# Optimization experiments

Measured on AMD Instinct MI355X. Metric: run time of the kernel, lower is better.

Reference implementation:

```python
import jax, jax.numpy as jnp
import numpy as np

BINS = 10

def setup_inputs() -> dict:
    key = jax.random.key(0)
    k1, k2, k3 = jax.random.split(key, 3)
    B, C, H, W = 16, 80, 128, 128
    # predictions strictly inside (0,1) so log(pre) / log(1-pre) are finite
    pre = jax.random.uniform(k1, (B, C, H, W), dtype=jnp.float32) * 0.998 + 1e-3
    u = jax.random.uniform(k2, (B, C, H, W), dtype=jnp.float32)
    gt = jnp.where(u > 0.99, jnp.float32(1.0), u * 0.5).astype(jnp.float32)
    # accumulated per-bin sample counts (GHM running stats); strictly positive
    acc_sum = jax.random.uniform(k3, (BINS,), dtype=jnp.float32) * 1e5 + 1e3
    return {"pre": pre, "gt": gt, "acc_sum": acc_sum}

def reference(pre, gt, acc_sum):
    bins = acc_sum.shape[0]
    tot = pre.size  # B*C*H*W, python int
    # gradient magnitude, detached (torch: .detach())
    g = jax.lax.stop_gradient(jnp.abs(pre - gt))
    # edges[i] = i/bins with edges[-1] += 1e-6, so bin(g) = min(floor(g*bins), bins-1)
    bin_idx = jnp.clip(jnp.floor(g * bins).astype(jnp.int32), 0, bins - 1)
    counts = jnp.zeros((bins,), jnp.float32).at[bin_idx].add(1.0)  # histogram
    nonempty = counts > 0
    n = jnp.sum(nonempty.astype(jnp.float32))  # number of non-empty bins
    w_per_bin = jnp.where(nonempty, tot / acc_sum, jnp.float32(0.0))
    weights = w_per_bin[bin_idx]                       # scatter-style weight assignment
    weights = jnp.where(n > 0, weights / n, weights)
    pos_mask = (gt == 1.0).astype(pre.dtype)
    neg_mask = 1.0 - pos_mask
    loss = (jnp.log(pre) * pos_mask + jnp.log1p(-pre) * neg_mask) * weights
    return jnp.sum(loss) / tot
```

## Files before the change

kernel.cpp:

```cpp
#include <hip/hip_runtime.h>

#define BINS 10
#define NTHR 256
#define MAXBLK 2048
#define UNROLL 5


__device__ __forceinline__ void ghm_elem(float pe, float te,
                                         const float* __restrict__ wtab,
                                         float& acc, unsigned int& mask) {
    float g = fabsf(pe - te);
    int bin = (int)(g * 10.0f);
    bin = bin > (BINS - 1) ? (BINS - 1) : bin;
    mask |= (1u << bin);
    float arg = (te == 1.0f) ? pe : (1.0f - pe);
    acc = fmaf(__log2f(arg), wtab[bin], acc);
}

__global__ __launch_bounds__(NTHR) void ghm_partial_kernel(
    const float* __restrict__ pre,
    const float* __restrict__ gt,
    const float* __restrict__ acc_sum,
    float* __restrict__ blk_sum,
    unsigned int* __restrict__ blk_mask,
    int n4,
    int tot)
{
    __shared__ float wtab[BINS];
    if (threadIdx.x < BINS)
        wtab[threadIdx.x] = 0.69314718055994531f / acc_sum[threadIdx.x];
    __syncthreads();

    float acc0 = 0.0f, acc1 = 0.0f;
    unsigned int mask = 0u;

    const float4* __restrict__ p4 = reinterpret_cast<const float4*>(pre);
    const float4* __restrict__ g4 = reinterpret_cast<const float4*>(gt);

    const int stride = gridDim.x * blockDim.x;
    int i = blockIdx.x * blockDim.x + threadIdx.x;

    for (; i + (UNROLL - 1) * stride < n4; i += UNROLL * stride) {
        float4 P[UNROLL], T[UNROLL];
#pragma unroll
        for (int u = 0; u < UNROLL; ++u) {
            P[u] = p4[i + u * stride];
            T[u] = g4[i + u * stride];
        }
#pragma unroll
        for (int u = 0; u < UNROLL; ++u) {
            ghm_elem(P[u].x, T[u].x, wtab, acc0, mask);
            ghm_elem(P[u].y, T[u].y, wtab, acc1, mask);
            ghm_elem(P[u].z, T[u].z, wtab, acc0, mask);
            ghm_elem(P[u].w, T[u].w, wtab, acc1, mask);
        }
    }
    for (; i < n4; i += stride) {
        float4 p = p4[i];
        float4 t = g4[i];
        ghm_elem(p.x, t.x, wtab, acc0, mask);
        ghm_elem(p.y, t.y, wtab, acc1, mask);
        ghm_elem(p.z, t.z, wtab, acc0, mask);
        ghm_elem(p.w, t.w, wtab, acc1, mask);
    }
    const int rs = n4 * 4;
    const int rem = tot - rs;
    if (blockIdx.x == 0 && (int)threadIdx.x < rem) {
        ghm_elem(pre[rs + threadIdx.x], gt[rs + threadIdx.x], wtab, acc0, mask);
    }

    float acc = acc0 + acc1;

#pragma unroll
    for (int off = 32; off >= 1; off >>= 1) {
        acc  += __shfl_down(acc, off, 64);
        mask |= (unsigned int)__shfl_down((int)mask, off, 64);
    }

    __shared__ float ls[4];
    __shared__ unsigned int lm[4];
    const int lane = threadIdx.x & 63;
    const int wave = threadIdx.x >> 6;
    if (lane == 0) { ls[wave] = acc; lm[wave] = mask; }
    __syncthreads();
    if (threadIdx.x == 0) {
        blk_sum[blockIdx.x]  = ls[0] + ls[1] + ls[2] + ls[3];
        blk_mask[blockIdx.x] = lm[0] | lm[1] | lm[2] | lm[3];
    }
}

__global__ __launch_bounds__(NTHR) void ghm_finalize_kernel(
    const float* __restrict__ blk_sum,
    const unsigned int* __restrict__ blk_mask,
    float* __restrict__ out,
    int nblk)
{
    float acc = 0.0f;
    unsigned int mask = 0u;
    for (int i = threadIdx.x; i < nblk; i += NTHR) {
        acc  += blk_sum[i];
        mask |= blk_mask[i];
    }
#pragma unroll
    for (int off = 32; off >= 1; off >>= 1) {
        acc  += __shfl_down(acc, off, 64);
        mask |= (unsigned int)__shfl_down((int)mask, off, 64);
    }
    __shared__ float ls[4];
    __shared__ unsigned int lm[4];
    const int lane = threadIdx.x & 63;
    const int wave = threadIdx.x >> 6;
    if (lane == 0) { ls[wave] = acc; lm[wave] = mask; }
    __syncthreads();
    if (threadIdx.x == 0) {
        float total = ls[0] + ls[1] + ls[2] + ls[3];
        unsigned int m = lm[0] | lm[1] | lm[2] | lm[3];
        int n = __popc(m & ((1u << BINS) - 1u));
        out[0] = (n > 0) ? (total / (float)n) : total;
    }
}

extern "C" void kernel_launch(void* const* d_in, const int* in_sizes, int n_in,
                              void* d_out, int out_size, void* d_ws, size_t ws_size,
                              hipStream_t stream) {
    const float* pre     = (const float*)d_in[0];
    const float* gt      = (const float*)d_in[1];
    const float* acc_sum = (const float*)d_in[2];
    float* out = (float*)d_out;

    const int tot = in_sizes[0];
    const int n4  = tot / 4;

    int blocks = (n4 + NTHR - 1) / NTHR;
    if (blocks > MAXBLK) blocks = MAXBLK;
    if (blocks < 1) blocks = 1;

    float* blk_sum = (float*)d_ws;
    unsigned int* blk_mask = (unsigned int*)((char*)d_ws + MAXBLK * sizeof(float));

    ghm_partial_kernel<<<blocks, NTHR, 0, stream>>>(
        pre, gt, acc_sum, blk_sum, blk_mask, n4, tot);
    ghm_finalize_kernel<<<1, NTHR, 0, stream>>>(
        blk_sum, blk_mask, out, blocks);
}
```

Baseline: 188.7 us.

## Use contiguous per-block chunks with nontemporal vector loads, drop manual unroll

Replaces the grid-stride loop, which was unrolled five ways, with contiguous per-block chunks walked by a simple strided loop. Loads go through nontemporal builtins on ext_vector float4 types, hinting that the streamed data need not stay in cache. This aims to improve DRAM locality and cut cache pollution. The cost is less memory-level parallelism per thread, since the explicit five-way unroll that kept ten loads in flight is gone.

```diff
diff --git a/kernel.cpp b/kernel.cpp
--- a/kernel.cpp
+++ b/kernel.cpp
@@ -3,7 +3,8 @@
 #define BINS 10
 #define NTHR 256
 #define MAXBLK 2048
-#define UNROLL 5
+
+typedef float v4f __attribute__((ext_vector_type(4)));
 
 
 __device__ __forceinline__ void ghm_elem(float pe, float te,
@@ -34,35 +35,23 @@
     float acc0 = 0.0f, acc1 = 0.0f;
     unsigned int mask = 0u;
 
-    const float4* __restrict__ p4 = reinterpret_cast<const float4*>(pre);
-    const float4* __restrict__ g4 = reinterpret_cast<const float4*>(gt);
+    const v4f* __restrict__ p4 = reinterpret_cast<const v4f*>(pre);
+    const v4f* __restrict__ g4 = reinterpret_cast<const v4f*>(gt);
 
-    const int stride = gridDim.x * blockDim.x;
-    int i = blockIdx.x * blockDim.x + threadIdx.x;
+    const int chunk = (n4 + gridDim.x - 1) / gridDim.x;
+    const int beg = blockIdx.x * chunk;
+    int end = beg + chunk;
+    if (end > n4) end = n4;
 
-    for (; i + (UNROLL - 1) * stride < n4; i += UNROLL * stride) {
-        float4 P[UNROLL], T[UNROLL];
-#pragma unroll
-        for (int u = 0; u < UNROLL; ++u) {
-            P[u] = p4[i + u * stride];
-            T[u] = g4[i + u * stride];
-        }
-#pragma unroll
-        for (int u = 0; u < UNROLL; ++u) {
-            ghm_elem(P[u].x, T[u].x, wtab, acc0, mask);
-            ghm_elem(P[u].y, T[u].y, wtab, acc1, mask);
-            ghm_elem(P[u].z, T[u].z, wtab, acc0, mask);
-            ghm_elem(P[u].w, T[u].w, wtab, acc1, mask);
-        }
-    }
-    for (; i < n4; i += stride) {
-        float4 p = p4[i];
-        float4 t = g4[i];
+    for (int i = beg + (int)threadIdx.x; i < end; i += NTHR) {
+        v4f p = __builtin_nontemporal_load(&p4[i]);
+        v4f t = __builtin_nontemporal_load(&g4[i]);
         ghm_elem(p.x, t.x, wtab, acc0, mask);
         ghm_elem(p.y, t.y, wtab, acc1, mask);
         ghm_elem(p.z, t.z, wtab, acc0, mask);
         ghm_elem(p.w, t.w, wtab, acc1, mask);
     }
+
     const int rs = n4 * 4;
     const int rem = tot - rs;
     if (blockIdx.x == 0 && (int)threadIdx.x < rem) {
```

Measured after the change: 171.6 us. 1.1x faster.
